# Kernel tuning notes

Hardware: AMD Instinct MI355X
Metric: run time of the kernel (lower is better)

Reference implementation:

```python
import jax, jax.numpy as jnp
import numpy as np

E = 8
TOP_K = 2
CAP_FACTOR = 1.25
MIN_CAP = 4
SCORE_SCALE = 1.0


def _ffn(x, w1, b1, w2, b2):
    # torch ExpertFFN: w2(gelu(w1(x))), exact (erf) gelu
    return jax.nn.gelu(x @ w1 + b1, approximate=False) @ w2 + b2


def setup_inputs() -> dict:
    key = jax.random.key(0)
    ks = jax.random.split(key, 6)
    B, S, D, I = 4, 2048, 1024, 4096
    std = 0.02
    return {
        'x': jax.random.normal(ks[0], (B, S, D), jnp.float32),
        'Wr': jax.random.normal(ks[1], (E, D), jnp.float32) * std,
        'W1': jax.random.normal(ks[2], (E, D, I), jnp.float32) * std,
        'b1': jnp.zeros((E, I), jnp.float32),
        'W2': jax.random.normal(ks[3], (E, I, D), jnp.float32) * std,
        'b2': jnp.zeros((E, D), jnp.float32),
        'fw1': jax.random.normal(ks[4], (D, I), jnp.float32) * std,
        'fb1': jnp.zeros((I,), jnp.float32),
        'fw2': jax.random.normal(ks[5], (I, D), jnp.float32) * std,
        'fb2': jnp.zeros((D,), jnp.float32),
    }


def reference(x, Wr, W1, b1, W2, b2, fw1, fb1, fw2, fb2):
    B, S, D = x.shape
    T = B * S
    x_flat = x.reshape(T, D)

    # ---- router ----
    logits = (x_flat @ Wr.T) * SCORE_SCALE            # [T, E]
    probs = jax.nn.softmax(logits, axis=-1)
    topk_scores, topk_experts = jax.lax.top_k(probs, TOP_K)   # [T,k]
    topk_scores = topk_scores / jnp.clip(
        topk_scores.sum(-1, keepdims=True), 1e-9, None)

    cap = max(int(CAP_FACTOR * (T * TOP_K / E)), MIN_CAP)

    # fallback output for all tokens (used only at overflow positions)
    y_fb = _ffn(x_flat, fw1, fb1, fw2, fb2)           # [T, D]

    y_flat = jnp.zeros_like(x_flat)
    fallback = jnp.zeros((T,), bool)  # route_threshold = 0 -> starts all False
    tok_ids = jnp.arange(T, dtype=jnp.int32)

    # sequential per-expert dispatch (matches torch loop semantics exactly,
    # including overwrite-on-overflow ordering)
    for e in range(E):
        match = topk_experts == e                     # [T, k]
        elig = match.any(-1) & ~fallback              # [T]
        pos = jnp.cumsum(elig) - 1                    # position among eligible, token order
        kept = elig & (pos < cap)
        overflow = elig & (pos >= cap)

        # capacity-limited gather: fixed-size [cap] buffer of token indices
        slot = jnp.where(kept, pos, cap)              # invalids dumped in slot `cap`
        buf = jnp.zeros((cap + 1,), jnp.int32).at[slot].set(tok_ids)
        vmask = jnp.zeros((cap + 1,), bool).at[slot].set(kept)
        idx = buf[:cap]                               # [cap]
        valid = vmask[:cap]                           # [cap]

        x_e = x_flat[idx]                             # [cap, D]
        y_e = _ffn(x_e, W1[e], b1[e], W2[e], b2[e])   # [cap, D]
        w_tok = (topk_scores * match).sum(-1)         # [T] (top-k experts distinct)
        w = jnp.where(valid, w_tok[idx], 0.0)         # [cap]
        y_flat = y_flat.at[idx].add(y_e * w[:, None])

        # overflow tokens: overwrite with dense fallback, mark as done
        y_flat = jnp.where(overflow[:, None], y_fb, y_flat)
        fallback = fallback | overflow

    return y_flat.reshape(B, S, D)
```

## Files before the change

kernel.cpp:

```cpp
#include <hip/hip_runtime.h>
#include <hip/hip_bf16.h>
#include <cstdint>
#include <cstddef>

#define TT 8192
#define DD 1024
#define II 4096
#define EE 8
#define CAP 2560

#define BM 128
#define BN 128
#define BK 32

typedef __attribute__((ext_vector_type(4))) float f32x4_t;
typedef __attribute__((ext_vector_type(8))) short bf16x8_t;

static __device__ __forceinline__ unsigned short f2bf(float f) {
    __hip_bfloat16 h = __float2bfloat16(f);
    return *reinterpret_cast<unsigned short*>(&h);
}
static __device__ __forceinline__ float geluf(float v) {
    return 0.5f * v * (1.0f + erff(v * 0.70710678118654752f));
}

static __device__ __forceinline__ void gl_lds16(const void* g, void* l) {
    __builtin_amdgcn_global_load_lds(
        (__attribute__((address_space(1))) unsigned int*)g,
        (__attribute__((address_space(3))) unsigned int*)l, 16, 0, 0);
}

__global__ __launch_bounds__(256) void cvt_x(
    const float* __restrict__ in, unsigned short* __restrict__ out) {
    int i = (blockIdx.x * 256 + threadIdx.x) * 8;
    float4 a = *(const float4*)(in + i);
    float4 b = *(const float4*)(in + i + 4);
    union { unsigned short s[8]; uint4 u; } pk;
    pk.s[0] = f2bf(a.x); pk.s[1] = f2bf(a.y); pk.s[2] = f2bf(a.z); pk.s[3] = f2bf(a.w);
    pk.s[4] = f2bf(b.x); pk.s[5] = f2bf(b.y); pk.s[6] = f2bf(b.z); pk.s[7] = f2bf(b.w);
    *(uint4*)(out + i) = pk.u;
}

__global__ __launch_bounds__(256) void transpose_cvt(
    const float* __restrict__ in, unsigned short* __restrict__ out, int R, int C) {
    __shared__ float tile[32][33];
    size_t mb = (size_t)blockIdx.z * (size_t)R * (size_t)C;
    in += mb; out += mb;
    int cb = blockIdx.x * 32, rb = blockIdx.y * 32;
    int tx = threadIdx.x, ty = threadIdx.y;
#pragma unroll
    for (int j = 0; j < 4; ++j)
        tile[ty + j * 8][tx] = in[(size_t)(rb + ty + j * 8) * C + cb + tx];
    __syncthreads();
#pragma unroll
    for (int j = 0; j < 4; ++j)
        out[(size_t)(cb + ty + j * 8) * R + rb + tx] = f2bf(tile[tx][ty + j * 8]);
}

__global__ __launch_bounds__(256) void router_kernel(
    const float* __restrict__ x, const float* __restrict__ Wr,
    int* __restrict__ e0a, int* __restrict__ e1a,
    float* __restrict__ w0a, float* __restrict__ w1a) {
    int t = blockIdx.x * 4 + (threadIdx.x >> 6);
    int lane = threadIdx.x & 63;
    const float* xr = x + (size_t)t * DD;
    float acc[EE];
#pragma unroll
    for (int e = 0; e < EE; ++e) acc[e] = 0.f;
    for (int c = 0; c < DD; c += 64) {
        float xv = xr[c + lane];
#pragma unroll
        for (int e = 0; e < EE; ++e) acc[e] += xv * Wr[e * DD + c + lane];
    }
#pragma unroll
    for (int e = 0; e < EE; ++e) {
        float v = acc[e];
#pragma unroll
        for (int off = 32; off > 0; off >>= 1) v += __shfl_xor(v, off, 64);
        acc[e] = v;
    }
    if (lane == 0) {
        int b0 = 0; float m0 = acc[0];
#pragma unroll
        for (int e = 1; e < EE; ++e) if (acc[e] > m0) { m0 = acc[e]; b0 = e; }
        int b1 = -1; float m1 = -3.4e38f;
#pragma unroll
        for (int e = 0; e < EE; ++e) if (e != b0 && acc[e] > m1) { m1 = acc[e]; b1 = e; }
        float w0 = 1.f / (1.f + expf(m1 - m0));
        e0a[t] = b0; e1a[t] = b1; w0a[t] = w0; w1a[t] = 1.f - w0;
    }
}

__global__ __launch_bounds__(1024) void assign_kernel(
    const int* __restrict__ e0a, const int* __restrict__ e1a,
    const float* __restrict__ w0a, const float* __restrict__ w1a,
    int* __restrict__ idxb, float* __restrict__ wslb,
    int* __restrict__ fbidx, int* __restrict__ counts) {
    __shared__ int wsum[16];
    __shared__ int ns[EE];
    const int t = threadIdx.x;
    const int lane = t & 63;
    const int wv = t >> 6;
    int e0v[8], e1v[8]; float w0v[8], w1v[8];
    bool fbv[8]; int sA[8], sB[8];
#pragma unroll
    for (int j = 0; j < 8; ++j) {
        int tok = t * 8 + j;
        e0v[j] = e0a[tok]; e1v[j] = e1a[tok];
        w0v[j] = w0a[tok]; w1v[j] = w1a[tok];
        fbv[j] = false; sA[j] = -1; sB[j] = -1;
    }
    for (int e = 0; e < EE; ++e) {
        int lp[8]; int c = 0; bool el[8];
#pragma unroll
        for (int j = 0; j < 8; ++j) {
            el[j] = (!fbv[j]) && (e0v[j] == e || e1v[j] == e);
            lp[j] = c; c += el[j] ? 1 : 0;
        }
        int incl = c;
#pragma unroll
        for (int off = 1; off < 64; off <<= 1) {
            int v = __shfl_up(incl, off, 64);
            if (lane >= off) incl += v;
        }
        if (lane == 63) wsum[wv] = incl;
        __syncthreads();
        int wbase = 0, total = 0;
#pragma unroll
        for (int u = 0; u < 16; ++u) {
            int v = wsum[u];
            total += v;
            if (u < wv) wbase += v;
        }
        int base = wbase + incl - c;
#pragma unroll
        for (int j = 0; j < 8; ++j) {
            if (el[j]) {
                int pos = base + lp[j];
                if (pos < CAP) {
                    int s = e * CAP + pos;
                    idxb[s] = t * 8 + j;
                    wslb[s] = (e0v[j] == e) ? w0v[j] : w1v[j];
                    if (sA[j] < 0) sA[j] = s; else sB[j] = s;
                } else {
                    fbv[j] = true;
                }
            }
        }
        if (t == 0) ns[e] = total < CAP ? total : CAP;
        __syncthreads();
    }
    for (int s = t; s < EE * CAP; s += 1024) {
        int e = s / CAP, pos = s - e * CAP;
        if (pos >= ns[e]) { idxb[s] = 0; wslb[s] = 0.f; }
    }
#pragma unroll
    for (int j = 0; j < 8; ++j) {
        if (fbv[j]) {
            if (sA[j] >= 0) wslb[sA[j]] = 0.f;
            if (sB[j] >= 0) wslb[sB[j]] = 0.f;
        }
    }
    int lp[8]; int c = 0;
#pragma unroll
    for (int j = 0; j < 8; ++j) { lp[j] = c; c += fbv[j] ? 1 : 0; }
    int incl = c;
#pragma unroll
    for (int off = 1; off < 64; off <<= 1) {
        int v = __shfl_up(incl, off, 64);
        if (lane >= off) incl += v;
    }
    if (lane == 63) wsum[wv] = incl;
    __syncthreads();
    int wbase = 0, total = 0;
#pragma unroll
    for (int u = 0; u < 16; ++u) {
        int v = wsum[u];
        total += v;
        if (u < wv) wbase += v;
    }
    int base = wbase + incl - c;
#pragma unroll
    for (int j = 0; j < 8; ++j)
        if (fbv[j]) fbidx[base + lp[j]] = t * 8 + j;
    for (int s = t; s < 4 * CAP; s += 1024)
        if (s >= total) fbidx[s] = 0;
    if (t == 0) {
        for (int e = 0; e < EE; ++e) counts[e] = ns[e];
        counts[EE] = total;
    }
}

template <int MODE>
__global__ __launch_bounds__(256) void gemm_kernel(
    const unsigned short* __restrict__ Abase,
    const unsigned short* __restrict__ Bt,
    const float* __restrict__ bias,
    unsigned short* __restrict__ Hout,
    float* __restrict__ dout,
    const int* __restrict__ idxp,
    const float* __restrict__ wslp,
    const int* __restrict__ counts,
    int e_base, int chunk_base) {
    constexpr bool IS_G1 = (MODE == 0 || MODE == 2);
    constexpr bool IS_EXPERT = (MODE == 0 || MODE == 1);
    constexpr int K = IS_G1 ? DD : II;

    const int z = blockIdx.z;
    const int e = e_base + z;
    const int ch0 = chunk_base + z * CAP;
    const int m_base = blockIdx.x * BM;
    const int n_base = blockIdx.y * BN;

    const int cnt = IS_EXPERT ? counts[e] : counts[EE];
    if (IS_EXPERT) { if (m_base >= cnt) return; }
    else           { if (ch0 + m_base >= cnt) return; }

    __shared__ alignas(16) unsigned short As[BM * BK];
    __shared__ alignas(16) unsigned short Bs[BN * BK];

    const int tid = threadIdx.x;
    const int lane = tid & 63;
    const int wv = tid >> 6;
    const int wm = (wv & 1) * 64;
    const int wn = (wv >> 1) * 64;
    const int l15 = lane & 15;
    const int quad = lane >> 4;

    const unsigned short* BtE;
    if (MODE == 0)      BtE = Bt + (size_t)e * II * DD;
    else if (MODE == 1) BtE = Bt + (size_t)e * DD * II;
    else                BtE = Bt;

    const int lrow = lane >> 2;
    const int kc = (lane & 3) ^ ((lrow >> 2) & 3);
    const unsigned short* aP[2];
    const unsigned short* bP[2];
#pragma unroll
    for (int p = 0; p < 2; ++p) {
        int r = wv * 32 + p * 16 + lrow;
        int slot = m_base + r;
        int arow;
        if (MODE == 0)      arow = idxp[e * CAP + slot];
        else if (MODE == 2) arow = idxp[ch0 + slot];
        else                arow = z * CAP + slot;
        aP[p] = Abase + (size_t)arow * K + kc * 8;
        int nrow = n_base + r;
        bP[p] = BtE + (size_t)nrow * K + kc * 8;
    }
    unsigned short* lA[2]; unsigned short* lB[2];
#pragma unroll
    for (int p = 0; p < 2; ++p) {
        lA[p] = &As[(wv * 32 + p * 16) * BK];
        lB[p] = &Bs[(wv * 32 + p * 16) * BK];
    }

    f32x4_t acc[4][4];
#pragma unroll
    for (int i = 0; i < 4; ++i)
#pragma unroll
        for (int j = 0; j < 4; ++j) acc[i][j] = (f32x4_t){0.f, 0.f, 0.f, 0.f};

    const int sw = (l15 >> 2) & 3;
    for (int k0 = 0; k0 < K; k0 += BK) {
        gl_lds16(aP[0], lA[0]); gl_lds16(aP[1], lA[1]);
        gl_lds16(bP[0], lB[0]); gl_lds16(bP[1], lB[1]);
        aP[0] += BK; aP[1] += BK; bP[0] += BK; bP[1] += BK;
        __syncthreads();
        bf16x8_t af[4], bfv[4];
#pragma unroll
        for (int i = 0; i < 4; ++i)
            af[i] = *(const bf16x8_t*)&As[(wm + i * 16 + l15) * BK + ((quad ^ sw) * 8)];
#pragma unroll
        for (int j = 0; j < 4; ++j)
            bfv[j] = *(const bf16x8_t*)&Bs[(wn + j * 16 + l15) * BK + ((quad ^ sw) * 8)];
#pragma unroll
        for (int i = 0; i < 4; ++i)
#pragma unroll
            for (int j = 0; j < 4; ++j)
                acc[i][j] = __builtin_amdgcn_mfma_f32_16x16x32_bf16(
                    af[i], bfv[j], acc[i][j], 0, 0, 0);
        __syncthreads();
    }

#pragma unroll
    for (int i = 0; i < 4; ++i) {
        const int mrow0 = wm + i * 16 + quad * 4;
#pragma unroll
        for (int j = 0; j < 4; ++j) {
            const int ncol = n_base + wn + j * 16 + l15;
            float bv;
            if (MODE == 0)      bv = bias[(size_t)e * II + ncol];
            else if (MODE == 1) bv = bias[(size_t)e * DD + ncol];
            else                bv = bias[ncol];
#pragma unroll
            for (int r = 0; r < 4; ++r) {
                const int slot = m_base + mrow0 + r;
                float v = acc[i][j][r] + bv;
                if (MODE == 0 || MODE == 2) {
                    Hout[(size_t)(z * CAP + slot) * II + ncol] = f2bf(geluf(v));
                } else if (MODE == 1) {
                    float w = wslp[e * CAP + slot];
                    if (w != 0.f) {
                        int tok = idxp[e * CAP + slot];
                        atomicAdd(&dout[(size_t)tok * DD + ncol], v * w);
                    }
                } else {
                    int rg = ch0 + slot;
                    if (rg < cnt) {
                        int tok = idxp[rg];
                        dout[(size_t)tok * DD + ncol] = v;
                    }
                }
            }
        }
    }
}

extern "C" void kernel_launch(void* const* d_in, const int* in_sizes, int n_in,
                              void* d_out, int out_size, void* d_ws, size_t ws_size,
                              hipStream_t stream) {
    const float* x   = (const float*)d_in[0];
    const float* Wr  = (const float*)d_in[1];
    const float* W1  = (const float*)d_in[2];
    const float* b1  = (const float*)d_in[3];
    const float* W2  = (const float*)d_in[4];
    const float* b2  = (const float*)d_in[5];
    const float* fw1 = (const float*)d_in[6];
    const float* fb1 = (const float*)d_in[7];
    const float* fw2 = (const float*)d_in[8];
    const float* fb2 = (const float*)d_in[9];
    float* out = (float*)d_out;

    char* ws = (char*)d_ws;
    size_t off = 0;
    auto alloc = [&](size_t bytes) -> void* {
        void* p = ws + off;
        off += (bytes + 255) & ~(size_t)255;
        return p;
    };
    unsigned short* W1t  = (unsigned short*)alloc((size_t)EE * DD * II * 2);
    unsigned short* W2t  = (unsigned short*)alloc((size_t)EE * II * DD * 2);
    unsigned short* fw1t = (unsigned short*)alloc((size_t)DD * II * 2);
    unsigned short* fw2t = (unsigned short*)alloc((size_t)II * DD * 2);
    unsigned short* xbf  = (unsigned short*)alloc((size_t)TT * DD * 2);
    int*   e0a   = (int*)alloc(TT * 4);
    int*   e1a   = (int*)alloc(TT * 4);
    float* w0a   = (float*)alloc(TT * 4);
    float* w1a   = (float*)alloc(TT * 4);
    int*   idxb  = (int*)alloc(EE * CAP * 4);
    float* wslb  = (float*)alloc(EE * CAP * 4);
    int*   fbidx = (int*)alloc(4 * CAP * 4);
    int*   counts = (int*)alloc(64);

    size_t perExpert = (size_t)CAP * II * 2;
    size_t remain = (ws_size > off) ? (ws_size - off) : 0;
    int G = (int)(remain / perExpert);
    if (G < 1) G = 1;
    if (G > EE) G = EE;
    unsigned short* H = (unsigned short*)(ws + off);

    hipMemsetAsync(d_out, 0, (size_t)TT * DD * sizeof(float), stream);

    cvt_x<<<TT * DD / (256 * 8), 256, 0, stream>>>(x, xbf);
    transpose_cvt<<<dim3(II / 32, DD / 32, EE), dim3(32, 8), 0, stream>>>(W1, W1t, DD, II);
    transpose_cvt<<<dim3(DD / 32, II / 32, EE), dim3(32, 8), 0, stream>>>(W2, W2t, II, DD);
    transpose_cvt<<<dim3(II / 32, DD / 32, 1),  dim3(32, 8), 0, stream>>>(fw1, fw1t, DD, II);
    transpose_cvt<<<dim3(DD / 32, II / 32, 1),  dim3(32, 8), 0, stream>>>(fw2, fw2t, II, DD);

    router_kernel<<<TT / 4, 256, 0, stream>>>(x, Wr, e0a, e1a, w0a, w1a);
    assign_kernel<<<1, 1024, 0, stream>>>(e0a, e1a, w0a, w1a, idxb, wslb, fbidx, counts);

    for (int eb = 0; eb < EE; eb += G) {
        int g = (EE - eb < G) ? (EE - eb) : G;
        gemm_kernel<0><<<dim3(CAP / BM, II / BN, g), 256, 0, stream>>>(
            xbf, W1t, b1, H, nullptr, idxb, wslb, counts, eb, 0);
        gemm_kernel<1><<<dim3(CAP / BM, DD / BN, g), 256, 0, stream>>>(
            H, W2t, b2, nullptr, out, idxb, wslb, counts, eb, 0);
    }
    if (G >= 4) {
        gemm_kernel<2><<<dim3(CAP / BM, II / BN, 4), 256, 0, stream>>>(
            xbf, fw1t, fb1, H, nullptr, fbidx, nullptr, counts, 0, 0);
        gemm_kernel<3><<<dim3(CAP / BM, DD / BN, 4), 256, 0, stream>>>(
            H, fw2t, fb2, nullptr, out, fbidx, nullptr, counts, 0, 0);
    } else {
        for (int c = 0; c < 4; ++c) {
            gemm_kernel<2><<<dim3(CAP / BM, II / BN, 1), 256, 0, stream>>>(
                xbf, fw1t, fb1, H, nullptr, fbidx, nullptr, counts, 0, c * CAP);
            gemm_kernel<3><<<dim3(CAP / BM, DD / BN, 1), 256, 0, stream>>>(
                H, fw2t, fb2, nullptr, out, fbidx, nullptr, counts, 0, c * CAP);
        }
    }
    (void)in_sizes; (void)n_in; (void)out_size;
}
```

Baseline: 955.6 us.

## Double-buffer GEMM LDS tiles, transpose MFMA output for vector epilogue, use tanh GELU

Adds a two-stage LDS ping-pong so the global-to-LDS load of the next K tile is issued while MFMAs run on the current one, leaving one barrier per iteration instead of two. The MFMA operands are swapped so each lane's four accumulator values lie along N, which lets the epilogue do float4 bias loads, ushort4 bf16 stores and float4 fallback stores, and load the token index and weight once per row. The exact erf GELU is replaced by a tanh approximation built from fast exp and reciprocal. That approximation departs from the reference's exact GELU and could affect tolerance, and the extra LDS buffer may lower occupancy.

```diff
diff --git a/kernel.cpp b/kernel.cpp
--- a/kernel.cpp
+++ b/kernel.cpp
@@ -20,8 +20,14 @@
     __hip_bfloat16 h = __float2bfloat16(f);
     return *reinterpret_cast<unsigned short*>(&h);
 }
-static __device__ __forceinline__ float geluf(float v) {
-    return 0.5f * v * (1.0f + erff(v * 0.70710678118654752f));
+
+static __device__ __forceinline__ float gelu_fast(float x) {
+    float y = 0.7978845608028654f * (x + 0.044715f * x * x * x);
+    float a = fabsf(y);
+    float e = __expf(2.0f * a);
+    float t = 1.0f - 2.0f * __builtin_amdgcn_rcpf(e + 1.0f);
+    t = copysignf(t, y);
+    return 0.5f * x * (1.0f + t);
 }
 
 static __device__ __forceinline__ void gl_lds16(const void* g, void* l) {
@@ -216,8 +222,8 @@
     if (IS_EXPERT) { if (m_base >= cnt) return; }
     else           { if (ch0 + m_base >= cnt) return; }
 
-    __shared__ alignas(16) unsigned short As[BM * BK];
-    __shared__ alignas(16) unsigned short Bs[BN * BK];
+    __shared__ alignas(16) unsigned short As[2][BM * BK];
+    __shared__ alignas(16) unsigned short Bs[2][BM * BK];
 
     const int tid = threadIdx.x;
     const int lane = tid & 63;
@@ -248,12 +254,14 @@
         int nrow = n_base + r;
         bP[p] = BtE + (size_t)nrow * K + kc * 8;
     }
-    unsigned short* lA[2]; unsigned short* lB[2];
-#pragma unroll
-    for (int p = 0; p < 2; ++p) {
-        lA[p] = &As[(wv * 32 + p * 16) * BK];
-        lB[p] = &Bs[(wv * 32 + p * 16) * BK];
-    }
+    unsigned short* lA[2][2]; unsigned short* lB[2][2];
+#pragma unroll
+    for (int b = 0; b < 2; ++b)
+#pragma unroll
+        for (int p = 0; p < 2; ++p) {
+            lA[b][p] = &As[b][(wv * 32 + p * 16) * BK];
+            lB[b][p] = &Bs[b][(wv * 32 + p * 16) * BK];
+        }
 
     f32x4_t acc[4][4];
 #pragma unroll
@@ -262,56 +270,76 @@
         for (int j = 0; j < 4; ++j) acc[i][j] = (f32x4_t){0.f, 0.f, 0.f, 0.f};
 
     const int sw = (l15 >> 2) & 3;
-    for (int k0 = 0; k0 < K; k0 += BK) {
-        gl_lds16(aP[0], lA[0]); gl_lds16(aP[1], lA[1]);
-        gl_lds16(bP[0], lB[0]); gl_lds16(bP[1], lB[1]);
-        aP[0] += BK; aP[1] += BK; bP[0] += BK; bP[1] += BK;
+    const int nit = K / BK;
+
+    gl_lds16(aP[0], lA[0][0]); gl_lds16(aP[1], lA[0][1]);
+    gl_lds16(bP[0], lB[0][0]); gl_lds16(bP[1], lB[0][1]);
+    aP[0] += BK; aP[1] += BK; bP[0] += BK; bP[1] += BK;
+
+    for (int it = 0; it < nit; ++it) {
         __syncthreads();
+        const int cb = it & 1;
+        if (it + 1 < nit) {
+            const int nb = cb ^ 1;
+            gl_lds16(aP[0], lA[nb][0]); gl_lds16(aP[1], lA[nb][1]);
+            gl_lds16(bP[0], lB[nb][0]); gl_lds16(bP[1], lB[nb][1]);
+            aP[0] += BK; aP[1] += BK; bP[0] += BK; bP[1] += BK;
+        }
+        const unsigned short* Ab = As[cb];
+        const unsigned short* Bb = Bs[cb];
         bf16x8_t af[4], bfv[4];
 #pragma unroll
         for (int i = 0; i < 4; ++i)
-            af[i] = *(const bf16x8_t*)&As[(wm + i * 16 + l15) * BK + ((quad ^ sw) * 8)];
+            af[i] = *(const bf16x8_t*)&Ab[(wm + i * 16 + l15) * BK + ((quad ^ sw) * 8)];
 #pragma unroll
         for (int j = 0; j < 4; ++j)
-            bfv[j] = *(const bf16x8_t*)&Bs[(wn + j * 16 + l15) * BK + ((quad ^ sw) * 8)];
+            bfv[j] = *(const bf16x8_t*)&Bb[(wn + j * 16 + l15) * BK + ((quad ^ sw) * 8)];
 #pragma unroll
         for (int i = 0; i < 4; ++i)
 #pragma unroll
             for (int j = 0; j < 4; ++j)
                 acc[i][j] = __builtin_amdgcn_mfma_f32_16x16x32_bf16(
-                    af[i], bfv[j], acc[i][j], 0, 0, 0);
-        __syncthreads();
-    }
-
+                    bfv[j], af[i], acc[i][j], 0, 0, 0);
+    }
+
+    const float* biasE;
+    if (MODE == 0)      biasE = bias + (size_t)e * II;
+    else if (MODE == 1) biasE = bias + (size_t)e * DD;
+    else                biasE = bias;
 #pragma unroll
     for (int i = 0; i < 4; ++i) {
-        const int mrow0 = wm + i * 16 + quad * 4;
+        const int slot = m_base + wm + i * 16 + l15;
+        int tok = 0; float w = 0.f; bool ok3 = false;
+        if (MODE == 1) { w = wslp[e * CAP + slot]; tok = idxp[e * CAP + slot]; }
+        if (MODE == 3) {
+            int rg = ch0 + slot;
+            ok3 = rg < cnt;
+            tok = ok3 ? idxp[rg] : 0;
+        }
 #pragma unroll
         for (int j = 0; j < 4; ++j) {
-            const int ncol = n_base + wn + j * 16 + l15;
-            float bv;
-            if (MODE == 0)      bv = bias[(size_t)e * II + ncol];
-            else if (MODE == 1) bv = bias[(size_t)e * DD + ncol];
-            else                bv = bias[ncol];
-#pragma unroll
-            for (int r = 0; r < 4; ++r) {
-                const int slot = m_base + mrow0 + r;
-                float v = acc[i][j][r] + bv;
-                if (MODE == 0 || MODE == 2) {
-                    Hout[(size_t)(z * CAP + slot) * II + ncol] = f2bf(geluf(v));
-                } else if (MODE == 1) {
-                    float w = wslp[e * CAP + slot];
-                    if (w != 0.f) {
-                        int tok = idxp[e * CAP + slot];
-                        atomicAdd(&dout[(size_t)tok * DD + ncol], v * w);
-                    }
-                } else {
-                    int rg = ch0 + slot;
-                    if (rg < cnt) {
-                        int tok = idxp[rg];
-                        dout[(size_t)tok * DD + ncol] = v;
-                    }
+            const int n0 = n_base + wn + j * 16 + quad * 4;
+            float4 bv = *(const float4*)&biasE[n0];
+            float v0 = acc[i][j][0] + bv.x;
+            float v1 = acc[i][j][1] + bv.y;
+            float v2 = acc[i][j][2] + bv.z;
+            float v3 = acc[i][j][3] + bv.w;
+            if (MODE == 0 || MODE == 2) {
+                ushort4 h;
+                h.x = f2bf(gelu_fast(v0)); h.y = f2bf(gelu_fast(v1));
+                h.z = f2bf(gelu_fast(v2)); h.w = f2bf(gelu_fast(v3));
+                *(ushort4*)&Hout[(size_t)(z * CAP + slot) * II + n0] = h;
+            } else if (MODE == 1) {
+                if (w != 0.f) {
+                    float* dp = &dout[(size_t)tok * DD + n0];
+                    atomicAdd(dp + 0, v0 * w);
+                    atomicAdd(dp + 1, v1 * w);
+                    atomicAdd(dp + 2, v2 * w);
+                    atomicAdd(dp + 3, v3 * w);
                 }
+            } else {
+                if (ok3)
+                    *(float4*)&dout[(size_t)tok * DD + n0] = make_float4(v0, v1, v2, v3);
             }
         }
     }
```

Measured after the change: 1.034 ms. 8.2% more time.
